# Optimization experiments

Measured on AMD Instinct MI355X. Metric: run time of the kernel, lower is better.

## Reference

```python
import jax, jax.numpy as jnp
import numpy as np

N = 40000      # total nodes in batched graph
E = 400000     # total edges
IN = 256       # input feature dim (n_dim / in_feats)
OUT = 256      # out_feats (DGL GatedGraphConv requires in_feats <= out_feats)
B = 256        # number of graphs in the batch
STEPS = 3      # GRU propagation steps per GatedGraphConv layer


def _gru_cell(m, h, Wih, Whh, bih, bhh):
    # torch.nn.GRUCell math
    gi = m @ Wih.T + bih          # [N, 3*OUT]
    gh = h @ Whh.T + bhh
    ir, iz, inn = jnp.split(gi, 3, axis=-1)
    hr, hz, hn = jnp.split(gh, 3, axis=-1)
    r = jax.nn.sigmoid(ir + hr)
    z = jax.nn.sigmoid(iz + hz)
    n = jnp.tanh(inn + r * hn)
    return (1.0 - z) * n + z * h


def _gated_graph_conv(h, src, dst, W, b, Wih, Whh, bih, bhh):
    # DGL GatedGraphConv with n_etypes=1: zero-pad to out_feats, then
    # n_steps of (per-etype linear -> sum messages over edges -> GRU update)
    if h.shape[1] < OUT:
        h = jnp.pad(h, ((0, 0), (0, OUT - h.shape[1])))
    for _ in range(STEPS):
        a = h @ W.T + b                                      # [N, OUT]
        m = jax.ops.segment_sum(a[src], dst, num_segments=N)  # gather/scatter
        h = _gru_cell(m, h, Wih, Whh, bih, bhh)
    return h


def _global_attention_pool(h, graph_ids, Wg, bg):
    gate = h @ Wg.T + bg                                       # [N, 1]
    gmax = jax.ops.segment_max(gate, graph_ids, num_segments=B)  # [B, 1]
    e = jnp.exp(gate - gmax[graph_ids])
    denom = jax.ops.segment_sum(e, graph_ids, num_segments=B)
    alpha = e / denom[graph_ids]                               # per-graph softmax
    return jax.ops.segment_sum(h * alpha, graph_ids, num_segments=B)  # [B, OUT]


def _forward(features, W0, b0, Wih0, Whh0, bih0, bhh0,
             W1, b1, Wih1, Whh1, bih1, bhh1, Wg, bg, Wo, bo,
             src, dst, graph_ids):
    # forward(): y = sigmoid(layer0(g, x)); y = sigmoid(layer1(g, y));
    # y = attention_pool(g, y); return sigmoid(output_layer(y))  (BCE branch)
    y = jax.nn.sigmoid(_gated_graph_conv(features, src, dst, W0, b0, Wih0, Whh0, bih0, bhh0))
    y = jax.nn.sigmoid(_gated_graph_conv(y, src, dst, W1, b1, Wih1, Whh1, bih1, bhh1))
    y = _global_attention_pool(y, graph_ids, Wg, bg)           # [B, OUT]
    return jax.nn.sigmoid(y @ Wo.T + bo)                        # [B, 1]


def setup_inputs() -> dict:
    key = jax.random.key(0)
    ks = jax.random.split(key, 20)
    s = lambda k, shape: (jax.random.normal(k, shape, jnp.float32) * 0.05)
    inp = {}
    inp["features"] = jax.random.normal(ks[0], (N, IN), jnp.float32)
    inp["src"] = jax.random.randint(ks[1], (E,), 0, N, jnp.int32)
    inp["dst"] = jax.random.randint(ks[2], (E,), 0, N, jnp.int32)
    inp["graph_ids"] = jnp.sort(jax.random.randint(ks[3], (N,), 0, B, jnp.int32))
    for li, off in ((0, 4), (1, 8)):
        inp[f"W{li}"] = s(ks[off], (OUT, OUT))
        inp[f"b{li}"] = jnp.zeros((OUT,), jnp.float32)
        inp[f"Wih{li}"] = s(ks[off + 1], (3 * OUT, OUT))
        inp[f"Whh{li}"] = s(ks[off + 2], (3 * OUT, OUT))
        inp[f"bih{li}"] = jnp.zeros((3 * OUT,), jnp.float32)
        inp[f"bhh{li}"] = jnp.zeros((3 * OUT,), jnp.float32)
    inp["Wg"] = s(ks[16], (1, OUT))
    inp["bg"] = jnp.zeros((1,), jnp.float32)
    inp["Wo"] = s(ks[17], (1, OUT))
    inp["bo"] = jnp.zeros((1,), jnp.float32)
    return inp


def reference(features, src, dst, graph_ids,
              W0, b0, Wih0, Whh0, bih0, bhh0,
              W1, b1, Wih1, Whh1, bih1, bhh1,
              Wg, bg, Wo, bo):
    return _forward(features, W0, b0, Wih0, Whh0, bih0, bhh0,
                    W1, b1, Wih1, Whh1, bih1, bhh1, Wg, bg, Wo, bo,
                    src, dst, graph_ids)
```

## Files before the change

kernel.cpp:

```cpp
#include <hip/hip_runtime.h>
#include <math.h>

#define NN 40000
#define EE 400000
#define BB 256

typedef __attribute__((ext_vector_type(8))) short short8;
typedef __attribute__((ext_vector_type(4))) float f32x4;
typedef __attribute__((address_space(1))) unsigned int glb_u32;
typedef __attribute__((address_space(3))) unsigned int lds_u32;

#define MFMA16 __builtin_amdgcn_mfma_f32_16x16x32_bf16

__device__ __forceinline__ float sigf(float x) { return 1.0f / (1.0f + __expf(-x)); }
__device__ __forceinline__ float tanhfast(float x) { return 2.0f / (1.0f + __expf(-2.0f * x)) - 1.0f; }
__device__ __forceinline__ unsigned short f2b(float f) {
    unsigned u = __float_as_uint(f);
    u += 0x7FFFu + ((u >> 16) & 1u);
    return (unsigned short)(u >> 16);
}
__device__ __forceinline__ float b2f(unsigned short h) { return __uint_as_float(((unsigned)h) << 16); }
__device__ __forceinline__ short8 ld8(const unsigned short* p) {
    return __builtin_bit_cast(short8, *(const uint4*)p);
}
__device__ __forceinline__ void gld_lds16(const void* g, void* l) {
    __builtin_amdgcn_global_load_lds((const glb_u32*)g, (lds_u32*)l, 16, 0, 0);
}

__global__ void k_f2b(const float* __restrict__ s, unsigned short* __restrict__ d, int n4) {
    int i = blockIdx.x * blockDim.x + threadIdx.x;
    if (i < n4) {
        float4 v = ((const float4*)s)[i];
        ushort4 o;
        o.x = f2b(v.x); o.y = f2b(v.y); o.z = f2b(v.z); o.w = f2b(v.w);
        ((ushort4*)d)[i] = o;
    }
}

__global__ __launch_bounds__(256) void k_wfuse(const float* __restrict__ Wih,
                                               const float* __restrict__ W,
                                               const float* __restrict__ b,
                                               unsigned short* __restrict__ Wf,
                                               float* __restrict__ vib) {
    int g = blockIdx.x;
    int c = threadIdx.x;
    __shared__ float row[256];
    __shared__ float red[256];
    row[c] = Wih[(size_t)g * 256 + c];
    __syncthreads();
    float acc = 0.f;
#pragma unroll 8
    for (int o = 0; o < 256; o++) acc += row[o] * W[(size_t)o * 256 + c];
    Wf[(size_t)g * 256 + c] = f2b(acc);
    red[c] = row[c] * b[c];
    __syncthreads();
    for (int off = 128; off; off >>= 1) {
        if (c < off) red[c] += red[c + off];
        __syncthreads();
    }
    if (c == 0) vib[g] = red[0];
}

__global__ void k_wpack(const unsigned short* __restrict__ Wf,
                        const float* __restrict__ Whh,
                        unsigned short* __restrict__ Wp) {
    int id = blockIdx.x * 256 + threadIdx.x;
    if (id >= 49152) return;
    int lane = id & 63;
    int t = (id >> 6) & 3;
    int q = (id >> 8) % 6;
    int bk = (id >> 8) / 6;
    int ks = bk & 7, bn_t = bk >> 3;
    int col = bn_t * 64 + t * 16 + (lane & 15);
    int k = ks * 32 + (lane >> 4) * 8;
    unsigned short o[8];
    if (q < 3) {
        const unsigned short* s = Wf + (size_t)(q * 256 + col) * 256 + k;
#pragma unroll
        for (int j = 0; j < 8; j++) o[j] = s[j];
    } else {
        const float* s = Whh + (size_t)((q - 3) * 256 + col) * 256 + k;
#pragma unroll
        for (int j = 0; j < 8; j++) o[j] = f2b(s[j]);
    }
    *(uint4*)(Wp + (size_t)id * 8) = *(const uint4*)o;
}

__global__ void k_zeroi(int* __restrict__ p, int n) {
    int i = blockIdx.x * blockDim.x + threadIdx.x;
    if (i < n) p[i] = 0;
}

__global__ void k_hist(const int* __restrict__ dst, int* __restrict__ cnt) {
    int e = blockIdx.x * blockDim.x + threadIdx.x;
    if (e < EE) atomicAdd(&cnt[dst[e]], 1);
}

__global__ __launch_bounds__(1024) void k_scanA(const int* __restrict__ cnt, int* __restrict__ rp,
                                                int* __restrict__ bsum) {
    __shared__ int sm[1024];
    int b = blockIdx.x, t = threadIdx.x;
    int i = b * 1024 + t;
    sm[t] = (i < NN) ? cnt[i] : 0;
    __syncthreads();
    for (int off = 1; off < 1024; off <<= 1) {
        int u = (t >= off) ? sm[t - off] : 0;
        __syncthreads();
        sm[t] += u;
        __syncthreads();
    }
    if (i < NN) rp[i + 1] = sm[t];
    if (t == 1023) bsum[b] = sm[1023];
}

__global__ void k_scanB(const int* __restrict__ bsum, int* __restrict__ boff, int* __restrict__ rp) {
    if (threadIdx.x == 0) {
        int run = 0;
        for (int k = 0; k < 40; k++) { boff[k] = run; run += bsum[k]; }
        rp[0] = 0;
    }
}

__global__ void k_scanC(int* __restrict__ rp, const int* __restrict__ boff) {
    int i = blockIdx.x * 256 + threadIdx.x;
    if (i < NN) rp[i + 1] += boff[i >> 10];
}

__global__ void k_fill(const int* __restrict__ src, const int* __restrict__ dst,
                       const int* __restrict__ rp, int* __restrict__ cur, int* __restrict__ cs) {
    int e = blockIdx.x * blockDim.x + threadIdx.x;
    if (e < EE) {
        int v = dst[e];
        int pos = rp[v] + atomicAdd(&cur[v], 1);
        cs[pos] = src[e];
    }
}

__device__ __forceinline__ void acc8(float* a, uint4 v) {
    a[0] += b2f((unsigned short)(v.x & 0xFFFF));
    a[1] += b2f((unsigned short)(v.x >> 16));
    a[2] += b2f((unsigned short)(v.y & 0xFFFF));
    a[3] += b2f((unsigned short)(v.y >> 16));
    a[4] += b2f((unsigned short)(v.z & 0xFFFF));
    a[5] += b2f((unsigned short)(v.z >> 16));
    a[6] += b2f((unsigned short)(v.w & 0xFFFF));
    a[7] += b2f((unsigned short)(v.w >> 16));
}

__global__ __launch_bounds__(256) void k_aggr(const unsigned short* __restrict__ Hb,
                                              const int* __restrict__ rp,
                                              const int* __restrict__ cs,
                                              unsigned short* __restrict__ Agg) {
    int v = blockIdx.x * 8 + (threadIdx.x >> 5);
    int hl = threadIdx.x & 31;
    int s = rp[v], e = rp[v + 1];
    float a[8] = {};
    int j = s;
    for (; j + 8 <= e; j += 8) {
        uint4 x0 = *(const uint4*)&Hb[(size_t)cs[j] * 256 + hl * 8];
        uint4 x1 = *(const uint4*)&Hb[(size_t)cs[j + 1] * 256 + hl * 8];
        uint4 x2 = *(const uint4*)&Hb[(size_t)cs[j + 2] * 256 + hl * 8];
        uint4 x3 = *(const uint4*)&Hb[(size_t)cs[j + 3] * 256 + hl * 8];
        uint4 x4 = *(const uint4*)&Hb[(size_t)cs[j + 4] * 256 + hl * 8];
        uint4 x5 = *(const uint4*)&Hb[(size_t)cs[j + 5] * 256 + hl * 8];
        uint4 x6 = *(const uint4*)&Hb[(size_t)cs[j + 6] * 256 + hl * 8];
        uint4 x7 = *(const uint4*)&Hb[(size_t)cs[j + 7] * 256 + hl * 8];
        acc8(a, x0); acc8(a, x1); acc8(a, x2); acc8(a, x3);
        acc8(a, x4); acc8(a, x5); acc8(a, x6); acc8(a, x7);
    }
    for (; j < e; j++) {
        uint4 x = *(const uint4*)&Hb[(size_t)cs[j] * 256 + hl * 8];
        acc8(a, x);
    }
    uint4 o;
    o.x = (unsigned)f2b(a[0]) | ((unsigned)f2b(a[1]) << 16);
    o.y = (unsigned)f2b(a[2]) | ((unsigned)f2b(a[3]) << 16);
    o.z = (unsigned)f2b(a[4]) | ((unsigned)f2b(a[5]) << 16);
    o.w = (unsigned)f2b(a[6]) | ((unsigned)f2b(a[7]) << 16);
    *(uint4*)&Agg[(size_t)v * 256 + hl * 8] = o;
}

__global__ __launch_bounds__(256, 3) void k_gru(const unsigned short* __restrict__ Mb,
                                                const unsigned short* __restrict__ Hb,
                                                const char* __restrict__ Wp,
                                                const float* __restrict__ bih,
                                                const float* __restrict__ bhh,
                                                const float* __restrict__ vib,
                                                const int* __restrict__ cnt,
                                                unsigned short* __restrict__ Hout, int fin) {
    __shared__ uint4 Wl[2][1536];
    const int tid = threadIdx.x;
    const int lane = tid & 63, wid = tid >> 6;
    const int wr = wid >> 1, wc = wid & 1;
    const int p = blockIdx.x;
    const int xcd = p & 7, rank = p >> 3;
    const int logical = (xcd < 4 ? xcd * 313 : 1252 + (xcd - 4) * 312) + rank;
    const int bm = (logical >> 2) * 64, bn_t = logical & 3, bn = bn_t * 64;
    const int l15 = lane & 15, lk = lane >> 4;

    const unsigned short* m0p = Mb + (size_t)(bm + wr * 32 + l15) * 256 + lk * 8;
    const unsigned short* m1p = m0p + 16 * 256;
    const unsigned short* h0p = Hb + (size_t)(bm + wr * 32 + l15) * 256 + lk * 8;
    const unsigned short* h1p = h0p + 16 * 256;

    const char* wbase = Wp + (size_t)bn_t * 8 * 24576;
    char* lds0 = (char*)&Wl[0][0];
    char* lds1 = (char*)&Wl[1][0];
    const int soff = wid * 1024 + lane * 16;

#define STAGE(b, ks)                                                        \
    {                                                                       \
        const char* gs = wbase + (ks) * 24576;                              \
        char* lb = (b) ? lds1 : lds0;                                       \
        _Pragma("unroll") for (int i = 0; i < 6; i++)                       \
            gld_lds16(gs + i * 4096 + soff, lb + i * 4096 + wid * 1024);    \
    }

    f32x4 acc[6][2][2] = {};
    short8 m0, m1, h0, h1, nm0, nm1, nh0, nh1;

    STAGE(0, 0);
    asm volatile("" ::: "memory");
    m0 = ld8(m0p); m1 = ld8(m1p); h0 = ld8(h0p); h1 = ld8(h1p);

    for (int ks = 0; ks < 8; ks++) {
        int cur = ks & 1;
        asm volatile("s_waitcnt vmcnt(4)" ::: "memory");
        __builtin_amdgcn_s_barrier();
        __builtin_amdgcn_sched_barrier(0);
        if (ks < 7) {
            STAGE(cur ^ 1, ks + 1);
            asm volatile("" ::: "memory");
            int ke = (ks + 1) * 32;
            nm0 = ld8(m0p + ke); nm1 = ld8(m1p + ke);
            nh0 = ld8(h0p + ke); nh1 = ld8(h1p + ke);
        }
        __builtin_amdgcn_s_setprio(1);
#pragma unroll
        for (int q = 0; q < 6; q++) {
            short8 b0 = __builtin_bit_cast(short8, Wl[cur][(q * 4 + wc * 2 + 0) * 64 + lane]);
            short8 b1 = __builtin_bit_cast(short8, Wl[cur][(q * 4 + wc * 2 + 1) * 64 + lane]);
            short8 a0 = q < 3 ? m0 : h0;
            short8 a1 = q < 3 ? m1 : h1;
            acc[q][0][0] = MFMA16(a0, b0, acc[q][0][0], 0, 0, 0);
            acc[q][1][0] = MFMA16(a1, b0, acc[q][1][0], 0, 0, 0);
            acc[q][0][1] = MFMA16(a0, b1, acc[q][0][1], 0, 0, 0);
            acc[q][1][1] = MFMA16(a1, b1, acc[q][1][1], 0, 0, 0);
        }
        __builtin_amdgcn_s_setprio(0);
        m0 = nm0; m1 = nm1; h0 = nh0; h1 = nh1;
    }
#undef STAGE

    const int lk4 = lk * 4;
#pragma unroll
    for (int f = 0; f < 2; f++)
#pragma unroll
        for (int t = 0; t < 2; t++) {
            int col = bn + wc * 32 + t * 16 + l15;
            float bi0 = bih[col], bi1 = bih[col + 256], bi2 = bih[col + 512];
            float bh0 = bhh[col], bh1 = bhh[col + 256], bh2 = bhh[col + 512];
            float v0 = vib[col], v1 = vib[col + 256], v2 = vib[col + 512];
#pragma unroll
            for (int r = 0; r < 4; r++) {
                int n = bm + wr * 32 + f * 16 + lk4 + r;
                float cf = (float)cnt[n];
                float ho = b2f(Hb[(size_t)n * 256 + col]);
                float irv = acc[0][f][t][r] + bi0 + cf * v0;
                float izv = acc[1][f][t][r] + bi1 + cf * v1;
                float inv = acc[2][f][t][r] + bi2 + cf * v2;
                float hrv = acc[3][f][t][r] + bh0;
                float hzv = acc[4][f][t][r] + bh1;
                float hnv = acc[5][f][t][r] + bh2;
                float rg = sigf(irv + hrv);
                float zg = sigf(izv + hzv);
                float nv = tanhfast(inv + rg * hnv);
                float v = (1.0f - zg) * nv + zg * ho;
                if (fin) v = sigf(v);
                Hout[(size_t)n * 256 + col] = f2b(v);
            }
        }
}

__global__ __launch_bounds__(256) void k_gate(const unsigned short* __restrict__ H,
                                              const float* __restrict__ Wg,
                                              const float* __restrict__ bg,
                                              float* __restrict__ gate) {
    int v = blockIdx.x * 4 + (threadIdx.x >> 6);
    int lane = threadIdx.x & 63;
    if (v >= NN) return;
    ushort4 hv = *(const ushort4*)&H[(size_t)v * 256 + lane * 4];
    float4 wv = *(const float4*)&Wg[lane * 4];
    float s = b2f(hv.x) * wv.x + b2f(hv.y) * wv.y + b2f(hv.z) * wv.z + b2f(hv.w) * wv.w;
    for (int off = 32; off; off >>= 1) s += __shfl_down(s, off);
    if (lane == 0) gate[v] = s + bg[0];
}

__global__ void k_bounds(const int* __restrict__ ids, int* __restrict__ gs, int* __restrict__ ge) {
    int b = threadIdx.x;
    int lo = 0, hi = NN;
    while (lo < hi) { int mid = (lo + hi) >> 1; if (ids[mid] < b) lo = mid + 1; else hi = mid; }
    gs[b] = lo;
    lo = 0; hi = NN;
    int key = b + 1;
    while (lo < hi) { int mid = (lo + hi) >> 1; if (ids[mid] < key) lo = mid + 1; else hi = mid; }
    ge[b] = lo;
}

__global__ __launch_bounds__(256) void k_pool(const unsigned short* __restrict__ H,
                                              const float* __restrict__ gate,
                                              const int* __restrict__ gs,
                                              const int* __restrict__ ge,
                                              float* __restrict__ pooled) {
    int b = blockIdx.x;
    int s = gs[b], e = ge[b];
    int t = threadIdx.x;
    __shared__ float red[256];
    __shared__ float wsh[256];
    float mx = -INFINITY;
    for (int n = s + t; n < e; n += 256) mx = fmaxf(mx, gate[n]);
    red[t] = mx;
    __syncthreads();
    for (int off = 128; off; off >>= 1) {
        if (t < off) red[t] = fmaxf(red[t], red[t + off]);
        __syncthreads();
    }
    mx = red[0];
    __syncthreads();
    float sm = 0.f;
    for (int n = s + t; n < e; n += 256) sm += __expf(gate[n] - mx);
    red[t] = sm;
    __syncthreads();
    for (int off = 128; off; off >>= 1) {
        if (t < off) red[t] += red[t + off];
        __syncthreads();
    }
    float denom = red[0];
    __syncthreads();
    float acc = 0.f;
    for (int c = s; c < e; c += 256) {
        int n = c + t;
        wsh[t] = (n < e) ? __expf(gate[n] - mx) / denom : 0.f;
        __syncthreads();
        int lim = e - c; if (lim > 256) lim = 256;
        for (int q = 0; q < lim; q++) acc += wsh[q] * b2f(H[(size_t)(c + q) * 256 + t]);
        __syncthreads();
    }
    pooled[(size_t)b * 256 + t] = acc;
}

__global__ void k_out(const float* __restrict__ pooled, const float* __restrict__ Wo,
                      const float* __restrict__ bo, float* __restrict__ out) {
    int b = blockIdx.x;
    int lane = threadIdx.x;
    float4 pv = *(const float4*)&pooled[(size_t)b * 256 + lane * 4];
    float4 wv = *(const float4*)&Wo[lane * 4];
    float s = pv.x * wv.x + pv.y * wv.y + pv.z * wv.z + pv.w * wv.w;
    for (int off = 32; off; off >>= 1) s += __shfl_down(s, off);
    if (lane == 0) out[b] = sigf(s + bo[0]);
}

extern "C" void kernel_launch(void* const* d_in, const int* in_sizes, int n_in,
                              void* d_out, int out_size, void* d_ws, size_t ws_size,
                              hipStream_t stream) {
    const float* features = (const float*)d_in[0];
    const int* src = (const int*)d_in[1];
    const int* dst = (const int*)d_in[2];
    const int* gids = (const int*)d_in[3];
    const float* W[2]   = {(const float*)d_in[4],  (const float*)d_in[10]};
    const float* bW[2]  = {(const float*)d_in[5],  (const float*)d_in[11]};
    const float* Wih[2] = {(const float*)d_in[6],  (const float*)d_in[12]};
    const float* Whh[2] = {(const float*)d_in[7],  (const float*)d_in[13]};
    const float* bih[2] = {(const float*)d_in[8],  (const float*)d_in[14]};
    const float* bhh[2] = {(const float*)d_in[9],  (const float*)d_in[15]};
    const float* Wg = (const float*)d_in[16];
    const float* bg = (const float*)d_in[17];
    const float* Wo = (const float*)d_in[18];
    const float* bo = (const float*)d_in[19];
    float* out = (float*)d_out;

    char* p = (char*)d_ws;
    auto alloc = [&](size_t bytes) {
        char* r = p;
        p += (bytes + 255) / 256 * 256;
        return r;
    };
    unsigned short* hbF = (unsigned short*)alloc((size_t)NN * 256 * 2);
    unsigned short* hA = (unsigned short*)alloc((size_t)NN * 256 * 2);
    unsigned short* hB = (unsigned short*)alloc((size_t)NN * 256 * 2);
    unsigned short* agg = (unsigned short*)alloc((size_t)NN * 256 * 2);
    unsigned short* Wfb[2], *Wpk[2];
    float* vib[2];
    for (int i = 0; i < 2; i++) {
        Wfb[i] = (unsigned short*)alloc((size_t)768 * 256 * 2);
        Wpk[i] = (unsigned short*)alloc((size_t)49152 * 16);
        vib[i] = (float*)alloc((size_t)768 * 4);
    }
    int* rp = (int*)alloc((size_t)(NN + 1) * 4);
    int* cnt = (int*)alloc((size_t)NN * 4);
    int* cur = (int*)alloc((size_t)NN * 4);
    int* cs = (int*)alloc((size_t)EE * 4);
    int* bsum = (int*)alloc(64 * 4);
    int* boff = (int*)alloc(64 * 4);
    float* gate = (float*)alloc((size_t)NN * 4);
    int* gsb = (int*)alloc((size_t)BB * 4);
    int* geb = (int*)alloc((size_t)BB * 4);
    float* pooled = (float*)alloc((size_t)BB * 256 * 4);

    k_f2b<<<(NN * 256 / 4 + 255) / 256, 256, 0, stream>>>(features, hbF, NN * 256 / 4);
    for (int i = 0; i < 2; i++) {
        k_wfuse<<<768, 256, 0, stream>>>(Wih[i], W[i], bW[i], Wfb[i], vib[i]);
        k_wpack<<<192, 256, 0, stream>>>(Wfb[i], Whh[i], Wpk[i]);
    }

    k_zeroi<<<(NN + 255) / 256, 256, 0, stream>>>(cnt, NN);
    k_zeroi<<<(NN + 255) / 256, 256, 0, stream>>>(cur, NN);
    k_hist<<<(EE + 255) / 256, 256, 0, stream>>>(dst, cnt);
    k_scanA<<<40, 1024, 0, stream>>>(cnt, rp, bsum);
    k_scanB<<<1, 64, 0, stream>>>(bsum, boff, rp);
    k_scanC<<<157, 256, 0, stream>>>(rp, boff);
    k_fill<<<(EE + 255) / 256, 256, 0, stream>>>(src, dst, rp, cur, cs);
    k_bounds<<<1, 256, 0, stream>>>(gids, gsb, geb);

    const unsigned short* hcur = hbF;
    unsigned short* hnext = hA;
    for (int li = 0; li < 2; li++) {
        for (int s = 0; s < 3; s++) {
            k_aggr<<<5000, 256, 0, stream>>>(hcur, rp, cs, agg);
            int fin = (s == 2) ? 1 : 0;
            k_gru<<<2500, 256, 0, stream>>>(agg, hcur, (const char*)Wpk[li], bih[li], bhh[li],
                                            vib[li], cnt, hnext, fin);
            hcur = hnext;
            hnext = (hnext == hA) ? hB : hA;
        }
    }
    k_gate<<<10000, 256, 0, stream>>>(hcur, Wg, bg, gate);
    k_pool<<<BB, 256, 0, stream>>>(hcur, gate, gsb, geb, pooled);
    k_out<<<BB, 64, 0, stream>>>(pooled, Wo, bo, out);
}
```

Measured before the change: 720.6 us.

## Load GRU weights directly from global into registers instead of LDS double-buffering

The GRU GEMM kernel drops its LDS double-buffered weight staging (global_load_lds plus barriers). Each wave now loads its B fragments straight from global memory into registers inside a fully unrolled K loop, and the launch bound is relaxed from 3 to 2 blocks per SM. This removes barrier and LDS traffic. In exchange, every wave fetches weights separately (the two wr waves duplicate them through L2), there is no explicit prefetch overlap, and register pressure rises.

```diff
diff --git a/kernel.cpp b/kernel.cpp
--- a/kernel.cpp
+++ b/kernel.cpp
@@ -7,8 +7,6 @@
 
 typedef __attribute__((ext_vector_type(8))) short short8;
 typedef __attribute__((ext_vector_type(4))) float f32x4;
-typedef __attribute__((address_space(1))) unsigned int glb_u32;
-typedef __attribute__((address_space(3))) unsigned int lds_u32;
 
 #define MFMA16 __builtin_amdgcn_mfma_f32_16x16x32_bf16
 
@@ -22,9 +20,6 @@
 __device__ __forceinline__ float b2f(unsigned short h) { return __uint_as_float(((unsigned)h) << 16); }
 __device__ __forceinline__ short8 ld8(const unsigned short* p) {
     return __builtin_bit_cast(short8, *(const uint4*)p);
-}
-__device__ __forceinline__ void gld_lds16(const void* g, void* l) {
-    __builtin_amdgcn_global_load_lds((const glb_u32*)g, (lds_u32*)l, 16, 0, 0);
 }
 
 __global__ void k_f2b(const float* __restrict__ s, unsigned short* __restrict__ d, int n4) {
@@ -180,15 +175,14 @@
     *(uint4*)&Agg[(size_t)v * 256 + hl * 8] = o;
 }
 
-__global__ __launch_bounds__(256, 3) void k_gru(const unsigned short* __restrict__ Mb,
+__global__ __launch_bounds__(256, 2) void k_gru(const unsigned short* __restrict__ Mb,
                                                 const unsigned short* __restrict__ Hb,
-                                                const char* __restrict__ Wp,
+                                                const unsigned short* __restrict__ Wp,
                                                 const float* __restrict__ bih,
                                                 const float* __restrict__ bhh,
                                                 const float* __restrict__ vib,
                                                 const int* __restrict__ cnt,
                                                 unsigned short* __restrict__ Hout, int fin) {
-    __shared__ uint4 Wl[2][1536];
     const int tid = threadIdx.x;
     const int lane = tid & 63, wid = tid >> 6;
     const int wr = wid >> 1, wc = wid & 1;
@@ -203,54 +197,34 @@
     const unsigned short* h0p = Hb + (size_t)(bm + wr * 32 + l15) * 256 + lk * 8;
     const unsigned short* h1p = h0p + 16 * 256;
 
-    const char* wbase = Wp + (size_t)bn_t * 8 * 24576;
-    char* lds0 = (char*)&Wl[0][0];
-    char* lds1 = (char*)&Wl[1][0];
-    const int soff = wid * 1024 + lane * 16;
-
-#define STAGE(b, ks)                                                        \
-    {                                                                       \
-        const char* gs = wbase + (ks) * 24576;                              \
-        char* lb = (b) ? lds1 : lds0;                                       \
-        _Pragma("unroll") for (int i = 0; i < 6; i++)                       \
-            gld_lds16(gs + i * 4096 + soff, lb + i * 4096 + wid * 1024);    \
-    }
+    const unsigned short* wp = Wp + (size_t)bn_t * 98304 + (size_t)(wc * 2) * 512 + lane * 8;
 
     f32x4 acc[6][2][2] = {};
-    short8 m0, m1, h0, h1, nm0, nm1, nh0, nh1;
-
-    STAGE(0, 0);
-    asm volatile("" ::: "memory");
-    m0 = ld8(m0p); m1 = ld8(m1p); h0 = ld8(h0p); h1 = ld8(h1p);
-
+
+#pragma unroll
     for (int ks = 0; ks < 8; ks++) {
-        int cur = ks & 1;
-        asm volatile("s_waitcnt vmcnt(4)" ::: "memory");
-        __builtin_amdgcn_s_barrier();
-        __builtin_amdgcn_sched_barrier(0);
-        if (ks < 7) {
-            STAGE(cur ^ 1, ks + 1);
-            asm volatile("" ::: "memory");
-            int ke = (ks + 1) * 32;
-            nm0 = ld8(m0p + ke); nm1 = ld8(m1p + ke);
-            nh0 = ld8(h0p + ke); nh1 = ld8(h1p + ke);
+        const unsigned short* wk = wp + ks * 12288;
+        const int ke = ks * 32;
+        short8 m0 = ld8(m0p + ke), m1 = ld8(m1p + ke);
+        short8 h0 = ld8(h0p + ke), h1 = ld8(h1p + ke);
+        short8 b[12];
+#pragma unroll
+        for (int q = 0; q < 6; q++) {
+            b[2 * q + 0] = ld8(wk + q * 2048);
+            b[2 * q + 1] = ld8(wk + q * 2048 + 512);
         }
         __builtin_amdgcn_s_setprio(1);
 #pragma unroll
         for (int q = 0; q < 6; q++) {
-            short8 b0 = __builtin_bit_cast(short8, Wl[cur][(q * 4 + wc * 2 + 0) * 64 + lane]);
-            short8 b1 = __builtin_bit_cast(short8, Wl[cur][(q * 4 + wc * 2 + 1) * 64 + lane]);
             short8 a0 = q < 3 ? m0 : h0;
             short8 a1 = q < 3 ? m1 : h1;
-            acc[q][0][0] = MFMA16(a0, b0, acc[q][0][0], 0, 0, 0);
-            acc[q][1][0] = MFMA16(a1, b0, acc[q][1][0], 0, 0, 0);
-            acc[q][0][1] = MFMA16(a0, b1, acc[q][0][1], 0, 0, 0);
-            acc[q][1][1] = MFMA16(a1, b1, acc[q][1][1], 0, 0, 0);
+            acc[q][0][0] = MFMA16(a0, b[2 * q + 0], acc[q][0][0], 0, 0, 0);
+            acc[q][1][0] = MFMA16(a1, b[2 * q + 0], acc[q][1][0], 0, 0, 0);
+            acc[q][0][1] = MFMA16(a0, b[2 * q + 1], acc[q][0][1], 0, 0, 0);
+            acc[q][1][1] = MFMA16(a1, b[2 * q + 1], acc[q][1][1], 0, 0, 0);
         }
         __builtin_amdgcn_s_setprio(0);
-        m0 = nm0; m1 = nm1; h0 = nh0; h1 = nh1;
-    }
-#undef STAGE
+    }
 
     const int lk4 = lk * 4;
 #pragma unroll
@@ -428,7 +402,7 @@
         for (int s = 0; s < 3; s++) {
             k_aggr<<<5000, 256, 0, stream>>>(hcur, rp, cs, agg);
             int fin = (s == 2) ? 1 : 0;
-            k_gru<<<2500, 256, 0, stream>>>(agg, hcur, (const char*)Wpk[li], bih[li], bhh[li],
+            k_gru<<<2500, 256, 0, stream>>>(agg, hcur, Wpk[li], bih[li], bhh[li],
                                             vib[li], cnt, hnext, fin);
             hcur = hnext;
             hnext = (hnext == hA) ? hB : hA;
```

Result: slower. 797.0 us (+10.6%).
